# Kernel optimization log

Hardware: AMD Instinct MI355X
Metric: run time of the kernel (lower is better)

The kernel has to match this reference:

```python
import jax, jax.numpy as jnp
import numpy as np

HEADS = 16
EMBD = 1024
D_K = EMBD // HEADS


def setup_inputs() -> dict:
    key = jax.random.key(0)
    ks = jax.random.split(key, 9)
    s = 1.0 / np.sqrt(EMBD)
    inp = {
        "x": jax.random.normal(ks[0], (4, 2048, EMBD), dtype=jnp.float32),
        "w_q": jax.random.normal(ks[1], (EMBD, EMBD), dtype=jnp.float32) * s,
        "b_q": jax.random.normal(ks[2], (EMBD,), dtype=jnp.float32) * 0.01,
        "w_k": jax.random.normal(ks[3], (EMBD, EMBD), dtype=jnp.float32) * s,
        "b_k": jax.random.normal(ks[4], (EMBD,), dtype=jnp.float32) * 0.01,
        "w_v": jax.random.normal(ks[5], (EMBD, EMBD), dtype=jnp.float32) * s,
        "b_v": jax.random.normal(ks[6], (EMBD,), dtype=jnp.float32) * 0.01,
        "w_o": jax.random.normal(ks[7], (EMBD, EMBD), dtype=jnp.float32) * s,
        "b_o": jax.random.normal(ks[8], (EMBD,), dtype=jnp.float32) * 0.01,
    }
    return inp


def reference(x, w_q, b_q, w_k, b_k, w_v, b_v, w_o, b_o):
    b, s, e = x.shape
    # Linear layers (torch Linear: x @ W^T + b; weights stored as [out,in] -> here [in,out] already? We store [in,out])
    q = x @ w_q + b_q
    k = x @ w_k + b_k
    v = x @ w_v + b_v
    # reshape to [b, h, s, d_k]
    qh = q.reshape(b, s, HEADS, D_K).transpose(0, 2, 1, 3)
    kh = k.reshape(b, s, HEADS, D_K).transpose(0, 2, 1, 3)
    vh = v.reshape(b, s, HEADS, D_K).transpose(0, 2, 1, 3)
    scores = jnp.einsum('bhqd,bhkd->bhqk', qh, kh) / jnp.sqrt(jnp.asarray(D_K, x.dtype))
    attn = jax.nn.softmax(scores, axis=-1)
    out = jnp.einsum('bhqk,bhkd->bhqd', attn, vh)
    merged = out.transpose(0, 2, 1, 3).reshape(b, s, e)
    return merged @ w_o + b_o
```

## Files before the change

kernel.cpp:

```cpp
#include <hip/hip_runtime.h>
#include <math.h>

#define B 4
#define S 2048
#define E 1024
#define H 16
#define DK 64
#define NROW (B * S)
#define NT (S / 64)

typedef _Float16 half_t;
typedef __attribute__((ext_vector_type(8))) _Float16 half8;
typedef __attribute__((ext_vector_type(4))) _Float16 half4;
typedef __attribute__((ext_vector_type(4))) float f32x4;

__device__ __forceinline__ void gload_lds16(const void* g, void* l) {
    __builtin_amdgcn_global_load_lds((__attribute__((address_space(1))) void*)(g),
                                     (__attribute__((address_space(3))) void*)(l), 16, 0, 0);
}

__device__ __forceinline__ float fast_exp2(float x) {
    return __builtin_amdgcn_exp2f(x);
}

__global__ __launch_bounds__(256)
void cast_x_kernel(const float* __restrict__ x, half_t* __restrict__ xh) {
    const size_t i = ((size_t)blockIdx.x * 256 + threadIdx.x) * 8;
    float4 a = *(const float4*)(x + i);
    float4 b = *(const float4*)(x + i + 4);
    half8 hv;
    hv[0] = (half_t)a.x; hv[1] = (half_t)a.y; hv[2] = (half_t)a.z; hv[3] = (half_t)a.w;
    hv[4] = (half_t)b.x; hv[5] = (half_t)b.y; hv[6] = (half_t)b.z; hv[7] = (half_t)b.w;
    *(half8*)(xh + i) = hv;
}

__global__ __launch_bounds__(256)
void cast_wT_kernel(const float* __restrict__ w0, const float* __restrict__ w1,
                    const float* __restrict__ w2, const float* __restrict__ w3,
                    half_t* __restrict__ o0, half_t* __restrict__ o1,
                    half_t* __restrict__ o2, half_t* __restrict__ o3) {
    __shared__ half_t Ts[64][72];
    const int z = blockIdx.z;
    const float* W = (z == 0) ? w0 : (z == 1) ? w1 : (z == 2) ? w2 : w3;
    half_t*      O = (z == 0) ? o0 : (z == 1) ? o1 : (z == 2) ? o2 : o3;
    const int t  = threadIdx.x;
    const int k0 = blockIdx.y * 64;
    const int n0 = blockIdx.x * 64;
    const int r  = t >> 2;
    const int c0 = (t & 3) * 16;
    const float* p = W + (size_t)(k0 + r) * E + n0 + c0;
    #pragma unroll
    for (int j = 0; j < 16; j += 4) {
        float4 v = *(const float4*)(p + j);
        Ts[c0 + j + 0][r] = (half_t)v.x;
        Ts[c0 + j + 1][r] = (half_t)v.y;
        Ts[c0 + j + 2][r] = (half_t)v.z;
        Ts[c0 + j + 3][r] = (half_t)v.w;
    }
    __syncthreads();
    half_t* q = O + (size_t)(n0 + r) * E + k0 + c0;
    *(uint4*)(q)     = *(const uint4*)&Ts[r][c0];
    *(uint4*)(q + 8) = *(const uint4*)&Ts[r][c0 + 8];
}

__global__ __launch_bounds__(256)
void gemm_qkv_kernel(const half_t* __restrict__ A, const half_t* __restrict__ Bt,
                     const float* __restrict__ b_q, const float* __restrict__ b_k,
                     const float* __restrict__ b_v,
                     half_t* __restrict__ Qh, half_t* __restrict__ Kh,
                     half_t* __restrict__ Vt) {
    __shared__ half_t As[128 * 32];
    __shared__ half_t Bs[128 * 32];
    const int t    = threadIdx.x;
    const int w    = t >> 6;
    const int lane = t & 63;
    const int ln   = t & 15;
    const int qd   = (t >> 4) & 3;
    const int bn0  = blockIdx.x * 128;
    const int bm0  = blockIdx.y * 128;
    const int wm   = (w & 1) * 64;
    const int wn   = (w >> 1) * 64;
    const int srow = lane >> 2;
    const int sch  = (lane & 3) * 8;

    f32x4 acc[4][4];
    #pragma unroll
    for (int mi = 0; mi < 4; ++mi)
        #pragma unroll
        for (int ni = 0; ni < 4; ++ni) acc[mi][ni] = (f32x4){0.f, 0.f, 0.f, 0.f};

    for (int k0 = 0; k0 < E; k0 += 32) {
        #pragma unroll
        for (int c = 0; c < 2; ++c) {
            const int rr = c * 64 + w * 16;
            gload_lds16(A  + (size_t)(bm0 + rr + srow) * E + k0 + sch, As + rr * 32);
            gload_lds16(Bt + (size_t)(bn0 + rr + srow) * E + k0 + sch, Bs + rr * 32);
        }
        __syncthreads();
        half8 af[4], bf[4];
        #pragma unroll
        for (int mi = 0; mi < 4; ++mi) af[mi] = *(const half8*)(As + (wm + mi * 16 + ln) * 32 + qd * 8);
        #pragma unroll
        for (int ni = 0; ni < 4; ++ni) bf[ni] = *(const half8*)(Bs + (wn + ni * 16 + ln) * 32 + qd * 8);
        #pragma unroll
        for (int mi = 0; mi < 4; ++mi)
            #pragma unroll
            for (int ni = 0; ni < 4; ++ni)
                acc[mi][ni] = __builtin_amdgcn_mfma_f32_16x16x32_f16(af[mi], bf[ni], acc[mi][ni], 0, 0, 0);
        __syncthreads();
    }

    const int route = bn0 >> 10;
    const int nloc0 = bn0 & 1023;
    const float* bp = (route == 0) ? b_q : (route == 1) ? b_k : b_v;
    float bv[4];
    #pragma unroll
    for (int ni = 0; ni < 4; ++ni) bv[ni] = bp[nloc0 + wn + ni * 16 + ln];

    if (route < 2) {
        half_t* Cst = (route == 0) ? Qh : Kh;
        #pragma unroll
        for (int mi = 0; mi < 4; ++mi)
            #pragma unroll
            for (int r = 0; r < 4; ++r) {
                const size_t row = (size_t)(bm0 + wm + mi * 16 + qd * 4 + r);
                #pragma unroll
                for (int ni = 0; ni < 4; ++ni)
                    Cst[row * E + nloc0 + wn + ni * 16 + ln] = (half_t)(acc[mi][ni][r] + bv[ni]);
            }
    } else {
        #pragma unroll
        for (int mi = 0; mi < 4; ++mi) {
            const int row0 = bm0 + wm + mi * 16 + qd * 4;
            const int bb   = row0 >> 11;
            const int sb   = row0 & (S - 1);
            #pragma unroll
            for (int ni = 0; ni < 4; ++ni) {
                const int vcol = nloc0 + wn + ni * 16 + ln;
                const int hh = vcol >> 6, dd = vcol & 63;
                half4 pk;
                #pragma unroll
                for (int r = 0; r < 4; ++r) pk[r] = (half_t)(acc[mi][ni][r] + bv[ni]);
                *(half4*)(Vt + ((size_t)(bb * H + hh) * DK + dd) * S + sb) = pk;
            }
        }
    }
}

__global__ __launch_bounds__(256)
void gemm_oproj_kernel(const half_t* __restrict__ A, const half_t* __restrict__ Bt,
                       const float* __restrict__ bias, float* __restrict__ Cout) {
    __shared__ half_t As[128 * 32];
    __shared__ half_t Bs[128 * 32];
    const int t    = threadIdx.x;
    const int w    = t >> 6;
    const int lane = t & 63;
    const int ln   = t & 15;
    const int qd   = (t >> 4) & 3;
    const int bn0  = blockIdx.x * 128;
    const int bm0  = blockIdx.y * 128;
    const int wm   = (w & 1) * 64;
    const int wn   = (w >> 1) * 64;
    const int srow = lane >> 2;
    const int sch  = (lane & 3) * 8;

    f32x4 acc[4][4];
    #pragma unroll
    for (int mi = 0; mi < 4; ++mi)
        #pragma unroll
        for (int ni = 0; ni < 4; ++ni) acc[mi][ni] = (f32x4){0.f, 0.f, 0.f, 0.f};

    for (int k0 = 0; k0 < E; k0 += 32) {
        #pragma unroll
        for (int c = 0; c < 2; ++c) {
            const int rr = c * 64 + w * 16;
            gload_lds16(A  + (size_t)(bm0 + rr + srow) * E + k0 + sch, As + rr * 32);
            gload_lds16(Bt + (size_t)(bn0 + rr + srow) * E + k0 + sch, Bs + rr * 32);
        }
        __syncthreads();
        half8 af[4], bf[4];
        #pragma unroll
        for (int mi = 0; mi < 4; ++mi) af[mi] = *(const half8*)(As + (wm + mi * 16 + ln) * 32 + qd * 8);
        #pragma unroll
        for (int ni = 0; ni < 4; ++ni) bf[ni] = *(const half8*)(Bs + (wn + ni * 16 + ln) * 32 + qd * 8);
        #pragma unroll
        for (int mi = 0; mi < 4; ++mi)
            #pragma unroll
            for (int ni = 0; ni < 4; ++ni)
                acc[mi][ni] = __builtin_amdgcn_mfma_f32_16x16x32_f16(af[mi], bf[ni], acc[mi][ni], 0, 0, 0);
        __syncthreads();
    }

    float bv[4];
    #pragma unroll
    for (int ni = 0; ni < 4; ++ni) bv[ni] = bias[bn0 + wn + ni * 16 + ln];
    #pragma unroll
    for (int mi = 0; mi < 4; ++mi)
        #pragma unroll
        for (int r = 0; r < 4; ++r) {
            const size_t row = (size_t)(bm0 + wm + mi * 16 + qd * 4 + r);
            #pragma unroll
            for (int ni = 0; ni < 4; ++ni)
                Cout[row * E + bn0 + wn + ni * 16 + ln] = acc[mi][ni][r] + bv[ni];
        }
}

__global__ __launch_bounds__(256)
void attn_kernel5(const half_t* __restrict__ Qg, const half_t* __restrict__ Kg,
                  const half_t* __restrict__ Vtg, half_t* __restrict__ CTX) {
    __shared__ half_t Kbuf[2][4096];
    __shared__ half_t Vbuf[2][4096];
    __shared__ half_t Pt[128][72];

    const int t    = threadIdx.x;
    const int w    = t >> 6;
    const int lane = t & 63;
    const int ln   = t & 15;
    const int qd   = (t >> 4) & 3;
    const int bh   = blockIdx.y;
    const int b    = bh >> 4;
    const int h    = bh & 15;
    const int s0   = blockIdx.x * 128;
    const int q0   = w * 32;

    half8 aq[2][2];
    #pragma unroll
    for (int mt = 0; mt < 2; ++mt)
        #pragma unroll
        for (int kd = 0; kd < 2; ++kd)
            aq[mt][kd] = *(const half8*)(Qg +
                (size_t)(b * S + s0 + q0 + mt * 16 + ln) * E + h * DK + kd * 32 + qd * 8);

    const half_t* kgp = Kg + (size_t)(b * S + w * 16 + ln) * E + h * DK + qd * 8;
    const half_t* vgp = Vtg + (size_t)(bh * DK + w * 16 + ln) * S + qd * 8;

    gload_lds16(kgp,      &Kbuf[0][(w * 2 + 0) * 512]);
    gload_lds16(kgp + 32, &Kbuf[0][(w * 2 + 1) * 512]);
    gload_lds16(vgp,      &Vbuf[0][(w * 2 + 0) * 512]);
    gload_lds16(vgp + 32, &Vbuf[0][(w * 2 + 1) * 512]);

    f32x4 oacc[2][4];
    #pragma unroll
    for (int mt = 0; mt < 2; ++mt)
        #pragma unroll
        for (int dt = 0; dt < 4; ++dt) oacc[mt][dt] = (f32x4){0.f, 0.f, 0.f, 0.f};
    f32x4 lfrag[2];
    lfrag[0] = (f32x4){0.f, 0.f, 0.f, 0.f};
    lfrag[1] = (f32x4){0.f, 0.f, 0.f, 0.f};

    half8 vone;
    #pragma unroll
    for (int j = 0; j < 8; ++j) vone[j] = (half_t)1;

    const float kexp  = 0.1803368731f;
    const float kbias = 7.2134752f;

    for (int kt = 0; kt < NT; ++kt) {
        const int cur = kt & 1;
        __syncthreads();

        if (kt + 1 < NT) {
            const half_t* kp = kgp + (size_t)(kt + 1) * 64 * E;
            const half_t* vp = vgp + (kt + 1) * 64;
            gload_lds16(kp,      &Kbuf[1 - cur][(w * 2 + 0) * 512]);
            gload_lds16(kp + 32, &Kbuf[1 - cur][(w * 2 + 1) * 512]);
            gload_lds16(vp,      &Vbuf[1 - cur][(w * 2 + 0) * 512]);
            gload_lds16(vp + 32, &Vbuf[1 - cur][(w * 2 + 1) * 512]);
        }

        half8 kf[4][2];
        #pragma unroll
        for (int ct = 0; ct < 4; ++ct)
            #pragma unroll
            for (int kd = 0; kd < 2; ++kd)
                kf[ct][kd] = *(const half8*)&Kbuf[cur][(ct * 2 + kd) * 512 + lane * 8];

        #pragma unroll
        for (int mt = 0; mt < 2; ++mt) {
            f32x4 sacc[4];
            #pragma unroll
            for (int ct = 0; ct < 4; ++ct) {
                f32x4 s = (f32x4){0.f, 0.f, 0.f, 0.f};
                s = __builtin_amdgcn_mfma_f32_16x16x32_f16(aq[mt][0], kf[ct][0], s, 0, 0, 0);
                s = __builtin_amdgcn_mfma_f32_16x16x32_f16(aq[mt][1], kf[ct][1], s, 0, 0, 0);
                sacc[ct] = s;
            }
            #pragma unroll
            for (int ct = 0; ct < 4; ++ct)
                #pragma unroll
                for (int r = 0; r < 4; ++r) {
                    const float pv = fast_exp2(fmaf(sacc[ct][r], kexp, -kbias));
                    Pt[q0 + mt * 16 + qd * 4 + r][ct * 16 + ln] = (half_t)pv;
                }
        }

        half8 pa[2][2], vf[4][2];
        #pragma unroll
        for (int mt = 0; mt < 2; ++mt)
            #pragma unroll
            for (int kq = 0; kq < 2; ++kq)
                pa[mt][kq] = *(const half8*)&Pt[q0 + mt * 16 + ln][kq * 32 + qd * 8];
        #pragma unroll
        for (int dt = 0; dt < 4; ++dt)
            #pragma unroll
            for (int kq = 0; kq < 2; ++kq)
                vf[dt][kq] = *(const half8*)&Vbuf[cur][(dt * 2 + kq) * 512 + lane * 8];

        #pragma unroll
        for (int mt = 0; mt < 2; ++mt) {
            lfrag[mt] = __builtin_amdgcn_mfma_f32_16x16x32_f16(pa[mt][0], vone, lfrag[mt], 0, 0, 0);
            lfrag[mt] = __builtin_amdgcn_mfma_f32_16x16x32_f16(pa[mt][1], vone, lfrag[mt], 0, 0, 0);
            #pragma unroll
            for (int dt = 0; dt < 4; ++dt) {
                oacc[mt][dt] = __builtin_amdgcn_mfma_f32_16x16x32_f16(pa[mt][0], vf[dt][0], oacc[mt][dt], 0, 0, 0);
                oacc[mt][dt] = __builtin_amdgcn_mfma_f32_16x16x32_f16(pa[mt][1], vf[dt][1], oacc[mt][dt], 0, 0, 0);
            }
        }
    }

    #pragma unroll
    for (int mt = 0; mt < 2; ++mt)
        #pragma unroll
        for (int r = 0; r < 4; ++r) {
            const float invl = 1.f / lfrag[mt][r];
            const size_t row = (size_t)(b * S + s0 + q0 + mt * 16 + qd * 4 + r);
            #pragma unroll
            for (int dt = 0; dt < 4; ++dt)
                CTX[row * E + h * DK + dt * 16 + ln] = (half_t)(oacc[mt][dt][r] * invl);
        }
}

extern "C" void kernel_launch(void* const* d_in, const int* in_sizes, int n_in,
                              void* d_out, int out_size, void* d_ws, size_t ws_size,
                              hipStream_t stream) {
    const float* x   = (const float*)d_in[0];
    const float* w_q = (const float*)d_in[1];
    const float* b_q = (const float*)d_in[2];
    const float* w_k = (const float*)d_in[3];
    const float* b_k = (const float*)d_in[4];
    const float* w_v = (const float*)d_in[5];
    const float* b_v = (const float*)d_in[6];
    const float* w_o = (const float*)d_in[7];
    const float* b_o = (const float*)d_in[8];
    float* out = (float*)d_out;

    half_t* xh  = (half_t*)d_ws;
    half_t* Wt3 = xh  + (size_t)NROW * E;
    half_t* WtO = Wt3 + (size_t)3 * E * E;
    half_t* Qh  = WtO + (size_t)E * E;
    half_t* Kh  = Qh  + (size_t)NROW * E;
    half_t* Vt  = Kh  + (size_t)NROW * E;
    half_t* CTX = Vt  + (size_t)NROW * E;

    cast_x_kernel<<<dim3(NROW * E / (256 * 8)), dim3(256), 0, stream>>>(x, xh);
    cast_wT_kernel<<<dim3(16, 16, 4), dim3(256), 0, stream>>>(
        w_q, w_k, w_v, w_o,
        Wt3, Wt3 + (size_t)E * E, Wt3 + (size_t)2 * E * E, WtO);

    gemm_qkv_kernel<<<dim3(3 * E / 128, NROW / 128), dim3(256), 0, stream>>>(
        xh, Wt3, b_q, b_k, b_v, Qh, Kh, Vt);

    attn_kernel5<<<dim3(S / 128, B * H), dim3(256), 0, stream>>>(Qh, Kh, Vt, CTX);

    gemm_oproj_kernel<<<dim3(E / 128, NROW / 128), dim3(256), 0, stream>>>(CTX, WtO, b_o, out);
}
```

Measured before the change: 334.0 us.

## Keep softmax probabilities in registers by transposing the QK^T MFMA

QK^T is now computed as K·Q^T, with the MFMA operands swapped, so each lane's score accumulator already matches the A-operand fragment layout needed by the P·V MFMA. The probabilities are therefore packed straight into half8 registers instead of going through the shared Pt array. The V tile load and read pattern are reorganised to fit this layout, and launch bounds now request 3 blocks per CU. This removes an LDS write, a barrier-free read-back and 18KB of shared memory per block, at the cost of split half4 V reads that may raise register pressure under the tighter occupancy bound.

```diff
diff --git a/kernel.cpp b/kernel.cpp
--- a/kernel.cpp
+++ b/kernel.cpp
@@ -205,12 +205,11 @@
         }
 }
 
-__global__ __launch_bounds__(256)
-void attn_kernel5(const half_t* __restrict__ Qg, const half_t* __restrict__ Kg,
+__global__ __launch_bounds__(256, 3)
+void attn_kernel6(const half_t* __restrict__ Qg, const half_t* __restrict__ Kg,
                   const half_t* __restrict__ Vtg, half_t* __restrict__ CTX) {
     __shared__ half_t Kbuf[2][4096];
     __shared__ half_t Vbuf[2][4096];
-    __shared__ half_t Pt[128][72];
 
     const int t    = threadIdx.x;
     const int w    = t >> 6;
@@ -232,12 +231,12 @@
                 (size_t)(b * S + s0 + q0 + mt * 16 + ln) * E + h * DK + kd * 32 + qd * 8);
 
     const half_t* kgp = Kg + (size_t)(b * S + w * 16 + ln) * E + h * DK + qd * 8;
-    const half_t* vgp = Vtg + (size_t)(bh * DK + w * 16 + ln) * S + qd * 8;
+    const half_t* vgp = Vtg + (size_t)(bh * DK + w * 16 + (lane & 7)) * S + (lane >> 3) * 8;
 
     gload_lds16(kgp,      &Kbuf[0][(w * 2 + 0) * 512]);
     gload_lds16(kgp + 32, &Kbuf[0][(w * 2 + 1) * 512]);
-    gload_lds16(vgp,      &Vbuf[0][(w * 2 + 0) * 512]);
-    gload_lds16(vgp + 32, &Vbuf[0][(w * 2 + 1) * 512]);
+    gload_lds16(vgp,                 &Vbuf[0][(w * 2 + 0) * 512]);
+    gload_lds16(vgp + (size_t)8 * S, &Vbuf[0][(w * 2 + 1) * 512]);
 
     f32x4 oacc[2][4];
     #pragma unroll
@@ -254,6 +253,8 @@
 
     const float kexp  = 0.1803368731f;
     const float kbias = 7.2134752f;
+
+    const int vrb = (ln >> 3) * 512 + (ln & 7) * 8 + (qd & 1) * 4 + (qd >> 1) * 64;
 
     for (int kt = 0; kt < NT; ++kt) {
         const int cur = kt & 1;
@@ -264,8 +265,8 @@
             const half_t* vp = vgp + (kt + 1) * 64;
             gload_lds16(kp,      &Kbuf[1 - cur][(w * 2 + 0) * 512]);
             gload_lds16(kp + 32, &Kbuf[1 - cur][(w * 2 + 1) * 512]);
-            gload_lds16(vp,      &Vbuf[1 - cur][(w * 2 + 0) * 512]);
-            gload_lds16(vp + 32, &Vbuf[1 - cur][(w * 2 + 1) * 512]);
+            gload_lds16(vp,                 &Vbuf[1 - cur][(w * 2 + 0) * 512]);
+            gload_lds16(vp + (size_t)8 * S, &Vbuf[1 - cur][(w * 2 + 1) * 512]);
         }
 
         half8 kf[4][2];
@@ -275,45 +276,44 @@
             for (int kd = 0; kd < 2; ++kd)
                 kf[ct][kd] = *(const half8*)&Kbuf[cur][(ct * 2 + kd) * 512 + lane * 8];
 
+        half8 vf[4][2];
+        const half_t* vb = &Vbuf[cur][vrb];
+        #pragma unroll
+        for (int dt = 0; dt < 4; ++dt)
+            #pragma unroll
+            for (int kq = 0; kq < 2; ++kq) {
+                union { half4 h4[2]; half8 h8; } u;
+                u.h4[0] = *(const half4*)(vb + dt * 1024 + kq * 256);
+                u.h4[1] = *(const half4*)(vb + dt * 1024 + kq * 256 + 128);
+                vf[dt][kq] = u.h8;
+            }
+
         #pragma unroll
         for (int mt = 0; mt < 2; ++mt) {
             f32x4 sacc[4];
             #pragma unroll
             for (int ct = 0; ct < 4; ++ct) {
-                f32x4 s = (f32x4){0.f, 0.f, 0.f, 0.f};
-                s = __builtin_amdgcn_mfma_f32_16x16x32_f16(aq[mt][0], kf[ct][0], s, 0, 0, 0);
-                s = __builtin_amdgcn_mfma_f32_16x16x32_f16(aq[mt][1], kf[ct][1], s, 0, 0, 0);
-                sacc[ct] = s;
-            }
-            #pragma unroll
-            for (int ct = 0; ct < 4; ++ct)
+                f32x4 sv = (f32x4){0.f, 0.f, 0.f, 0.f};
+                sv = __builtin_amdgcn_mfma_f32_16x16x32_f16(kf[ct][0], aq[mt][0], sv, 0, 0, 0);
+                sv = __builtin_amdgcn_mfma_f32_16x16x32_f16(kf[ct][1], aq[mt][1], sv, 0, 0, 0);
+                sacc[ct] = sv;
+            }
+            half8 pa[2];
+            #pragma unroll
+            for (int kq = 0; kq < 2; ++kq)
                 #pragma unroll
-                for (int r = 0; r < 4; ++r) {
-                    const float pv = fast_exp2(fmaf(sacc[ct][r], kexp, -kbias));
-                    Pt[q0 + mt * 16 + qd * 4 + r][ct * 16 + ln] = (half_t)pv;
+                for (int j = 0; j < 8; ++j) {
+                    const int ct = kq * 2 + (j >> 2);
+                    const int r  = j & 3;
+                    pa[kq][j] = (half_t)fast_exp2(fmaf(sacc[ct][r], kexp, -kbias));
                 }
-        }
-
-        half8 pa[2][2], vf[4][2];
-        #pragma unroll
-        for (int mt = 0; mt < 2; ++mt)
-            #pragma unroll
-            for (int kq = 0; kq < 2; ++kq)
-                pa[mt][kq] = *(const half8*)&Pt[q0 + mt * 16 + ln][kq * 32 + qd * 8];
-        #pragma unroll
-        for (int dt = 0; dt < 4; ++dt)
-            #pragma unroll
-            for (int kq = 0; kq < 2; ++kq)
-                vf[dt][kq] = *(const half8*)&Vbuf[cur][(dt * 2 + kq) * 512 + lane * 8];
-
-        #pragma unroll
-        for (int mt = 0; mt < 2; ++mt) {
-            lfrag[mt] = __builtin_amdgcn_mfma_f32_16x16x32_f16(pa[mt][0], vone, lfrag[mt], 0, 0, 0);
-            lfrag[mt] = __builtin_amdgcn_mfma_f32_16x16x32_f16(pa[mt][1], vone, lfrag[mt], 0, 0, 0);
+
+            lfrag[mt] = __builtin_amdgcn_mfma_f32_16x16x32_f16(pa[0], vone, lfrag[mt], 0, 0, 0);
+            lfrag[mt] = __builtin_amdgcn_mfma_f32_16x16x32_f16(pa[1], vone, lfrag[mt], 0, 0, 0);
             #pragma unroll
             for (int dt = 0; dt < 4; ++dt) {
-                oacc[mt][dt] = __builtin_amdgcn_mfma_f32_16x16x32_f16(pa[mt][0], vf[dt][0], oacc[mt][dt], 0, 0, 0);
-                oacc[mt][dt] = __builtin_amdgcn_mfma_f32_16x16x32_f16(pa[mt][1], vf[dt][1], oacc[mt][dt], 0, 0, 0);
+                oacc[mt][dt] = __builtin_amdgcn_mfma_f32_16x16x32_f16(pa[0], vf[dt][0], oacc[mt][dt], 0, 0, 0);
+                oacc[mt][dt] = __builtin_amdgcn_mfma_f32_16x16x32_f16(pa[1], vf[dt][1], oacc[mt][dt], 0, 0, 0);
             }
         }
     }
@@ -360,7 +360,7 @@
     gemm_qkv_kernel<<<dim3(3 * E / 128, NROW / 128), dim3(256), 0, stream>>>(
         xh, Wt3, b_q, b_k, b_v, Qh, Kh, Vt);
 
-    attn_kernel5<<<dim3(S / 128, B * H), dim3(256), 0, stream>>>(Qh, Kh, Vt, CTX);
+    attn_kernel6<<<dim3(S / 128, B * H), dim3(256), 0, stream>>>(Qh, Kh, Vt, CTX);
 
     gemm_oproj_kernel<<<dim3(E / 128, NROW / 128), dim3(256), 0, stream>>>(CTX, WtO, b_o, out);
 }
```

After: 288.7 us. -13.6%, faster.
